# Kernel tuning notes

Hardware: AMD Instinct MI355X
Metric: run time of the kernel (lower is better)

The kernel has to match this reference:

```python
import jax, jax.numpy as jnp
import numpy as np

GRID = (32, 32)       # SOM grid shape
INPUT_DIM = 512
BATCH = 16384
TAU = 0.5             # softmax temperature
EPS = 1e-8


def setup_inputs() -> dict:
    key = jax.random.key(0)
    k1, k2 = jax.random.split(key)
    x = jax.random.normal(k1, (BATCH, INPUT_DIM), dtype=jnp.float32)
    # glorot_uniform for shape (*GRID, INPUT_DIM): fan_in = 32*32, fan_out = 512
    fan_in, fan_out = GRID[0] * GRID[1], INPUT_DIM
    limit = float(np.sqrt(6.0 / (fan_in + fan_out)))
    weights_map = jax.random.uniform(
        k2, (*GRID, INPUT_DIM), dtype=jnp.float32, minval=-limit, maxval=limit
    )
    return {"x": x, "weights_map": weights_map}


def reference(x, weights_map):
    """SoftSOM forward: squared distances -> per-dimension softmax -> soft reconstruction."""
    B, D = x.shape
    gh, gw = GRID
    w_flat = weights_map.reshape(gh * gw, D)  # [N, D]
    d2 = (
        jnp.sum(x * x, axis=-1, keepdims=True)           # [B,1]
        + jnp.sum(w_flat * w_flat, axis=-1)[None, :]     # [1,N]
        - 2.0 * (x @ w_flat.T)                           # [B,N]
    )
    logits = (-d2 / TAU).reshape(B, gh, gw)
    # per-dimension softmax: softmax along each grid axis, combined multiplicatively
    s_rows = jax.nn.softmax(logits, axis=1)   # softmax over grid dim 0
    s_cols = jax.nn.softmax(logits, axis=2)   # softmax over grid dim 1
    a = s_rows * s_cols
    a = a / (jnp.sum(a, axis=(1, 2), keepdims=True) + EPS)  # renormalize over grid
    # soft reconstruction: weighted sum of prototypes
    y = jnp.einsum("bij,ijd->bd", a, weights_map)  # [B, D]
    return y
```

## Files before the change

kernel.cpp:

```cpp
#include <hip/hip_runtime.h>
#include <hip/hip_bf16.h>
#include <stdint.h>

#define B_SZ 16384
#define D_SZ 512
#define N_SZ 1024

using f16x8 = __attribute__((ext_vector_type(8))) _Float16;
using f16x4 = __attribute__((ext_vector_type(4))) _Float16;
using f32x4 = __attribute__((ext_vector_type(4))) float;

typedef unsigned int u32_as1 __attribute__((address_space(1)));
typedef unsigned int u32_as3 __attribute__((address_space(3)));

__device__ __forceinline__ void gload16(const void* g, void* lds_base) {
    __builtin_amdgcn_global_load_lds((const u32_as1*)g, (u32_as3*)lds_base, 16, 0, 0);
}

__global__ __launch_bounds__(256) void prep(
    const float* __restrict__ W, const float* __restrict__ X,
    _Float16* __restrict__ wh, _Float16* __restrict__ wt,
    float* __restrict__ ww, _Float16* __restrict__ xh) {
    __shared__ float part[4];
    const int bid = blockIdx.x;
    const int t = threadIdx.x;
    if (bid < N_SZ) {
        const int n = bid;
        const float2 v = *reinterpret_cast<const float2*>(&W[(size_t)n * D_SZ + t * 2]);
        _Float16 h0 = (_Float16)v.x, h1 = (_Float16)v.y;
        wh[(size_t)n * D_SZ + t * 2] = h0;
        wh[(size_t)n * D_SZ + t * 2 + 1] = h1;
        wt[(size_t)(t * 2) * N_SZ + n] = h0;
        wt[(size_t)(t * 2 + 1) * N_SZ + n] = h1;
        float s = v.x * v.x + v.y * v.y;
        for (int o = 32; o; o >>= 1) s += __shfl_xor(s, o);
        if ((t & 63) == 0) part[t >> 6] = s;
        __syncthreads();
        if (t == 0) ww[n] = part[0] + part[1] + part[2] + part[3];
    } else {
        const int b2 = bid - N_SZ;
        const int chunk = (b2 & 7) * 512 + (b2 >> 3);
        const size_t idx = ((size_t)chunk * 256 + t) * 8;
        const float4 a = *reinterpret_cast<const float4*>(&X[idx]);
        const float4 b = *reinterpret_cast<const float4*>(&X[idx + 4]);
        f16x8 h = {(_Float16)a.x, (_Float16)a.y, (_Float16)a.z, (_Float16)a.w,
                   (_Float16)b.x, (_Float16)b.y, (_Float16)b.z, (_Float16)b.w};
        *reinterpret_cast<f16x8*>(&xh[idx]) = h;
    }
}

__global__ __launch_bounds__(256, 3) void gemm1(
    const _Float16* __restrict__ xh, const _Float16* __restrict__ wh,
    const float* __restrict__ ww, _Float16* __restrict__ L16) {
    __shared__ _Float16 smem[16384];
    const int tid = threadIdx.x;
    const int wid = tid >> 6, lane = tid & 63;
    const int raw = blockIdx.y * 8 + blockIdx.x;
    const int wsw = (raw & 7) * 128 + (raw >> 3);
    const int bn0 = (wsw & 7) * 128;
    const int bm0 = (wsw >> 3) * 128;
    const int m0 = (wid >> 1) * 64, n0 = (wid & 1) * 64;
    const int rA = lane & 15;
    const int cbr = (lane >> 4) * 16;
    const int rswz = ((rA >> 1) & 3) << 4;

    const int br0 = (wid * 2) * 16 + (lane >> 2);
    const int br1 = (wid * 2 + 1) * 16 + (lane >> 2);
    const int sg0 = ((lane & 3) ^ ((br0 >> 1) & 3)) * 8;
    const int sg1 = ((lane & 3) ^ ((br1 >> 1) & 3)) * 8;
    const int bdst0 = (wid * 2) * 1024;
    const int bdst1 = (wid * 2 + 1) * 1024;
    char* const As_b = (char*)smem;
    char* const Bs_b = (char*)smem + 16384;

    f32x4 acc[4][4];
    for (int mi = 0; mi < 4; ++mi)
        for (int ni = 0; ni < 4; ++ni) acc[mi][ni] = (f32x4){0.f, 0.f, 0.f, 0.f};

    gload16(&xh[(size_t)(bm0 + br0) * D_SZ + sg0], As_b + bdst0);
    gload16(&xh[(size_t)(bm0 + br1) * D_SZ + sg1], As_b + bdst1);
    gload16(&wh[(size_t)(bn0 + br0) * D_SZ + sg0], Bs_b + bdst0);
    gload16(&wh[(size_t)(bn0 + br1) * D_SZ + sg1], Bs_b + bdst1);
    __syncthreads();

    int cur = 0;
    for (int kt = 0; kt < 16; ++kt) {
        const int nxt = cur ^ 1;
        if (kt < 15) {
            const int gk = (kt + 1) * 32;
            gload16(&xh[(size_t)(bm0 + br0) * D_SZ + gk + sg0], As_b + nxt * 8192 + bdst0);
            gload16(&xh[(size_t)(bm0 + br1) * D_SZ + gk + sg1], As_b + nxt * 8192 + bdst1);
            gload16(&wh[(size_t)(bn0 + br0) * D_SZ + gk + sg0], Bs_b + nxt * 8192 + bdst0);
            gload16(&wh[(size_t)(bn0 + br1) * D_SZ + gk + sg1], Bs_b + nxt * 8192 + bdst1);
        }
        f16x8 af[4], bf[4];
        for (int mi = 0; mi < 4; ++mi)
            af[mi] = *reinterpret_cast<const f16x8*>(
                As_b + cur * 8192 + (m0 + mi * 16 + rA) * 64 + (cbr ^ rswz));
        for (int ni = 0; ni < 4; ++ni)
            bf[ni] = *reinterpret_cast<const f16x8*>(
                Bs_b + cur * 8192 + (n0 + ni * 16 + rA) * 64 + (cbr ^ rswz));
        for (int mi = 0; mi < 4; ++mi)
            for (int ni = 0; ni < 4; ++ni)
                acc[mi][ni] = __builtin_amdgcn_mfma_f32_16x16x32_f16(af[mi], bf[ni], acc[mi][ni], 0, 0, 0);
        __syncthreads();
        cur = nxt;
    }

    for (int mi = 0; mi < 4; ++mi)
        for (int ni = 0; ni < 4; ++ni) {
            const int ln = n0 + ni * 16 + rA;
            const float wwn = ww[bn0 + ln];
            const int lm = m0 + mi * 16 + (lane >> 4) * 4;
            const f32x4 a = acc[mi][ni];
            for (int r = 0; r < 4; ++r)
                smem[(lm + r) * 128 + ln] = (_Float16)(4.f * a[r] - 2.f * wwn);
        }
    __syncthreads();
    for (int c = 0; c < 8; ++c) {
        const int idx = c * 2048 + tid * 8;
        const int row = idx >> 7, col = idx & 127;
        const f16x8 v = *reinterpret_cast<const f16x8*>(&smem[idx]);
        *reinterpret_cast<f16x8*>(&L16[(size_t)(bm0 + row) * N_SZ + bn0 + col]) = v;
    }
}

__global__ __launch_bounds__(256) void softsm(_Float16* __restrict__ L16) {
    __shared__ float4 spart[4][8];
    __shared__ float mpart[4];
    __shared__ float Tp[4];
    const int t = threadIdx.x;
    const int w = t >> 6, lane = t & 63;
    const int g8 = t & 7;
    const int bid = blockIdx.x;
    const size_t row = (size_t)((bid & 7) * 2048 + (bid >> 3));
    const f16x4 lv = *reinterpret_cast<const f16x4*>(&L16[row * N_SZ + (size_t)t * 4]);
    const float v0 = (float)lv[0], v1 = (float)lv[1], v2 = (float)lv[2], v3 = (float)lv[3];

    float m = fmaxf(fmaxf(v0, v1), fmaxf(v2, v3));
    for (int o = 32; o; o >>= 1) m = fmaxf(m, __shfl_xor(m, o));
    if (lane == 0) mpart[w] = m;
    __syncthreads();
    m = fmaxf(fmaxf(mpart[0], mpart[1]), fmaxf(mpart[2], mpart[3]));

    const float u0 = __expf(v0 - m), u1 = __expf(v1 - m);
    const float u2 = __expf(v2 - m), u3 = __expf(v3 - m);
    float rs = (u0 + u1) + (u2 + u3);
    rs += __shfl_xor(rs, 1); rs += __shfl_xor(rs, 2); rs += __shfl_xor(rs, 4);
    float s0 = u0, s1 = u1, s2 = u2, s3 = u3;
    for (int o = 8; o <= 32; o <<= 1) {
        s0 += __shfl_xor(s0, o); s1 += __shfl_xor(s1, o);
        s2 += __shfl_xor(s2, o); s3 += __shfl_xor(s3, o);
    }
    if (lane < 8) spart[w][lane] = make_float4(s0, s1, s2, s3);
    __syncthreads();
    {
        const float4 q0 = spart[0][g8], q1 = spart[1][g8], q2 = spart[2][g8], q3 = spart[3][g8];
        s0 = (q0.x + q1.x) + (q2.x + q3.x);
        s1 = (q0.y + q1.y) + (q2.y + q3.y);
        s2 = (q0.z + q1.z) + (q2.z + q3.z);
        s3 = (q0.w + q1.w) + (q2.w + q3.w);
    }
    const float irs = __builtin_amdgcn_rcpf(rs);
    const float t0 = u0 * u0 * irs * __builtin_amdgcn_rcpf(s0);
    const float t1 = u1 * u1 * irs * __builtin_amdgcn_rcpf(s1);
    const float t2 = u2 * u2 * irs * __builtin_amdgcn_rcpf(s2);
    const float t3 = u3 * u3 * irs * __builtin_amdgcn_rcpf(s3);
    float sT = (t0 + t1) + (t2 + t3);
    for (int o = 1; o <= 32; o <<= 1) sT += __shfl_xor(sT, o);
    if (lane == 0) Tp[w] = sT;
    __syncthreads();
    const float T = (Tp[0] + Tp[1]) + (Tp[2] + Tp[3]);
    const float inv = __builtin_amdgcn_rcpf(T + 1e-8f);
    f16x4 o16 = {(_Float16)(t0 * inv), (_Float16)(t1 * inv),
                 (_Float16)(t2 * inv), (_Float16)(t3 * inv)};
    *reinterpret_cast<f16x4*>(&L16[row * N_SZ + (size_t)t * 4]) = o16;
}

__global__ __launch_bounds__(256, 3) void gemm2(
    const _Float16* __restrict__ a16, const _Float16* __restrict__ wt,
    float* __restrict__ Y) {
    __shared__ _Float16 As[2 * 128 * 32];
    __shared__ _Float16 Bs[2 * 128 * 32];
    const int tid = threadIdx.x;
    const int wid = tid >> 6, lane = tid & 63;
    const int raw = blockIdx.y * 4 + blockIdx.x;
    const int wsw = (raw & 7) * 64 + (raw >> 3);
    const int bn0 = (wsw & 3) * 128;
    const int bm0 = (wsw >> 2) * 128;
    const int m0 = (wid >> 1) * 64, n0 = (wid & 1) * 64;
    const int rA = lane & 15;
    const int cbr = (lane >> 4) * 16;
    const int rswz = ((rA >> 1) & 3) << 4;

    const int br0 = (wid * 2) * 16 + (lane >> 2);
    const int br1 = (wid * 2 + 1) * 16 + (lane >> 2);
    const int sg0 = ((lane & 3) ^ ((br0 >> 1) & 3)) * 8;
    const int sg1 = ((lane & 3) ^ ((br1 >> 1) & 3)) * 8;
    const int bdst0 = (wid * 2) * 1024;
    const int bdst1 = (wid * 2 + 1) * 1024;
    char* const As_b = (char*)As;
    char* const Bs_b = (char*)Bs;

    f32x4 acc[4][4];
    for (int mi = 0; mi < 4; ++mi)
        for (int ni = 0; ni < 4; ++ni) acc[mi][ni] = (f32x4){0.f, 0.f, 0.f, 0.f};

    gload16(&a16[(size_t)(bm0 + br0) * N_SZ + sg0], As_b + bdst0);
    gload16(&a16[(size_t)(bm0 + br1) * N_SZ + sg1], As_b + bdst1);
    gload16(&wt[(size_t)(bn0 + br0) * N_SZ + sg0], Bs_b + bdst0);
    gload16(&wt[(size_t)(bn0 + br1) * N_SZ + sg1], Bs_b + bdst1);
    __syncthreads();

    int cur = 0;
    for (int kt = 0; kt < 32; ++kt) {
        const int nxt = cur ^ 1;
        if (kt < 31) {
            const int gk = (kt + 1) * 32;
            gload16(&a16[(size_t)(bm0 + br0) * N_SZ + gk + sg0], As_b + nxt * 8192 + bdst0);
            gload16(&a16[(size_t)(bm0 + br1) * N_SZ + gk + sg1], As_b + nxt * 8192 + bdst1);
            gload16(&wt[(size_t)(bn0 + br0) * N_SZ + gk + sg0], Bs_b + nxt * 8192 + bdst0);
            gload16(&wt[(size_t)(bn0 + br1) * N_SZ + gk + sg1], Bs_b + nxt * 8192 + bdst1);
        }
        f16x8 af[4], bf[4];
        for (int mi = 0; mi < 4; ++mi)
            af[mi] = *reinterpret_cast<const f16x8*>(
                As_b + cur * 8192 + (m0 + mi * 16 + rA) * 64 + (cbr ^ rswz));
        for (int ni = 0; ni < 4; ++ni)
            bf[ni] = *reinterpret_cast<const f16x8*>(
                Bs_b + cur * 8192 + (n0 + ni * 16 + rA) * 64 + (cbr ^ rswz));
        for (int mi = 0; mi < 4; ++mi)
            for (int ni = 0; ni < 4; ++ni)
                acc[mi][ni] = __builtin_amdgcn_mfma_f32_16x16x32_f16(af[mi], bf[ni], acc[mi][ni], 0, 0, 0);
        __syncthreads();
        cur = nxt;
    }
    for (int mi = 0; mi < 4; ++mi)
        for (int ni = 0; ni < 4; ++ni) {
            const int dd = bn0 + n0 + ni * 16 + rA;
            const int bb = bm0 + m0 + mi * 16 + (lane >> 4) * 4;
            const f32x4 a = acc[mi][ni];
            for (int r = 0; r < 4; ++r)
                Y[(size_t)(bb + r) * D_SZ + dd] = a[r];
        }
}

extern "C" void kernel_launch(void* const* d_in, const int* in_sizes, int n_in,
                              void* d_out, int out_size, void* d_ws, size_t ws_size,
                              hipStream_t stream) {
    (void)in_sizes; (void)n_in; (void)out_size; (void)ws_size;
    const float* X = (const float*)d_in[0];
    const float* W = (const float*)d_in[1];
    float* Y = (float*)d_out;
    char* ws = (char*)d_ws;

    _Float16* L16 = (_Float16*)ws;
    _Float16* wh  = (_Float16*)(ws + (size_t)32 * 1024 * 1024);
    _Float16* wt  = (_Float16*)(ws + (size_t)33 * 1024 * 1024);
    float*    ww  = (float*)   (ws + (size_t)34 * 1024 * 1024);
    _Float16* xh  = (_Float16*)(ws + (size_t)34 * 1024 * 1024 + 4096);

    prep<<<N_SZ + 4096, 256, 0, stream>>>(W, X, wh, wt, ww, xh);
    gemm1<<<dim3(N_SZ / 128, B_SZ / 128), 256, 0, stream>>>(xh, wh, ww, L16);
    softsm<<<B_SZ, 256, 0, stream>>>(L16);
    gemm2<<<dim3(D_SZ / 128, B_SZ / 128), 256, 0, stream>>>(L16, wt, Y);
}
```

Measured before the change: 99.54 us.

## Tile weight transpose through LDS, process two rows per softmax block, raise occupancy

The weight prep path now uses 32 blocks, each covering 32 prototypes. Each block computes the squared norms, writes the fp16 copy with 16-byte stores, and transposes through padded, swizzled LDS so the transposed weights are also written with coalesced 16-byte stores instead of scattered 2-byte writes. The softmax kernel handles two rows per 512-thread block, which halves the block count. Both GEMMs raise their launch-bounds occupancy hint from 3 to 4 blocks, which may force register spills.

```diff
diff --git a/kernel.cpp b/kernel.cpp
--- a/kernel.cpp
+++ b/kernel.cpp
@@ -15,30 +15,79 @@
 
 __device__ __forceinline__ void gload16(const void* g, void* lds_base) {
     __builtin_amdgcn_global_load_lds((const u32_as1*)g, (u32_as3*)lds_base, 16, 0, 0);
+}
+
+__device__ __forceinline__ unsigned short f16bits(_Float16 h) {
+    return __builtin_bit_cast(unsigned short, h);
 }
 
 __global__ __launch_bounds__(256) void prep(
     const float* __restrict__ W, const float* __restrict__ X,
     _Float16* __restrict__ wh, _Float16* __restrict__ wt,
     float* __restrict__ ww, _Float16* __restrict__ xh) {
-    __shared__ float part[4];
     const int bid = blockIdx.x;
     const int t = threadIdx.x;
-    if (bid < N_SZ) {
-        const int n = bid;
-        const float2 v = *reinterpret_cast<const float2*>(&W[(size_t)n * D_SZ + t * 2]);
-        _Float16 h0 = (_Float16)v.x, h1 = (_Float16)v.y;
-        wh[(size_t)n * D_SZ + t * 2] = h0;
-        wh[(size_t)n * D_SZ + t * 2 + 1] = h1;
-        wt[(size_t)(t * 2) * N_SZ + n] = h0;
-        wt[(size_t)(t * 2 + 1) * N_SZ + n] = h1;
-        float s = v.x * v.x + v.y * v.y;
-        for (int o = 32; o; o >>= 1) s += __shfl_xor(s, o);
-        if ((t & 63) == 0) part[t >> 6] = s;
+    if (bid < 32) {
+        __shared__ unsigned int cells[512 * 17];
+        const int n0 = bid * 32;
+        const int np = t >> 4;
+        const int dc = t & 15;
+        const int na = n0 + 2 * np, nb = na + 1;
+        const int d0 = dc * 32;
+        float va[32], vb[32];
+#pragma unroll
+        for (int i = 0; i < 8; ++i) {
+            *reinterpret_cast<float4*>(&va[i * 4]) =
+                *reinterpret_cast<const float4*>(&W[(size_t)na * D_SZ + d0 + i * 4]);
+            *reinterpret_cast<float4*>(&vb[i * 4]) =
+                *reinterpret_cast<const float4*>(&W[(size_t)nb * D_SZ + d0 + i * 4]);
+        }
+        float sa = 0.f, sb = 0.f;
+#pragma unroll
+        for (int i = 0; i < 32; ++i) { sa += va[i] * va[i]; sb += vb[i] * vb[i]; }
+        sa += __shfl_xor(sa, 1); sa += __shfl_xor(sa, 2);
+        sa += __shfl_xor(sa, 4); sa += __shfl_xor(sa, 8);
+        sb += __shfl_xor(sb, 1); sb += __shfl_xor(sb, 2);
+        sb += __shfl_xor(sb, 4); sb += __shfl_xor(sb, 8);
+        if (dc == 0) { ww[na] = sa; ww[nb] = sb; }
+        _Float16 ha[32], hb[32];
+#pragma unroll
+        for (int i = 0; i < 32; ++i) { ha[i] = (_Float16)va[i]; hb[i] = (_Float16)vb[i]; }
+        unsigned int pa[16], pb[16];
+#pragma unroll
+        for (int j = 0; j < 16; ++j) {
+            pa[j] = (unsigned)f16bits(ha[2 * j]) | ((unsigned)f16bits(ha[2 * j + 1]) << 16);
+            pb[j] = (unsigned)f16bits(hb[2 * j]) | ((unsigned)f16bits(hb[2 * j + 1]) << 16);
+        }
+        unsigned int* whU = reinterpret_cast<unsigned int*>(wh);
+#pragma unroll
+        for (int j = 0; j < 4; ++j) {
+            *reinterpret_cast<uint4*>(&whU[((size_t)na * D_SZ + d0) / 2 + j * 4]) =
+                make_uint4(pa[j * 4], pa[j * 4 + 1], pa[j * 4 + 2], pa[j * 4 + 3]);
+            *reinterpret_cast<uint4*>(&whU[((size_t)nb * D_SZ + d0) / 2 + j * 4]) =
+                make_uint4(pb[j * 4], pb[j * 4 + 1], pb[j * 4 + 2], pb[j * 4 + 3]);
+        }
+#pragma unroll
+        for (int k = 0; k < 32; ++k) {
+            const int d = d0 + k;
+            const unsigned u = (unsigned)f16bits(ha[k]) | ((unsigned)f16bits(hb[k]) << 16);
+            cells[d * 17 + (np ^ ((d >> 5) & 15))] = u;
+        }
         __syncthreads();
-        if (t == 0) ww[n] = part[0] + part[1] + part[2] + part[3];
+        for (int rr = 0; rr < 2; ++rr) {
+            const int d = 2 * t + rr;
+            const int px = (d >> 5) & 15;
+            unsigned int buf[16];
+#pragma unroll
+            for (int j = 0; j < 16; ++j) buf[j] = cells[d * 17 + (j ^ px)];
+            unsigned int* wtU = reinterpret_cast<unsigned int*>(wt);
+#pragma unroll
+            for (int j = 0; j < 4; ++j)
+                *reinterpret_cast<uint4*>(&wtU[((size_t)d * N_SZ + n0) / 2 + j * 4]) =
+                    make_uint4(buf[j * 4], buf[j * 4 + 1], buf[j * 4 + 2], buf[j * 4 + 3]);
+        }
     } else {
-        const int b2 = bid - N_SZ;
+        const int b2 = bid - 32;
         const int chunk = (b2 & 7) * 512 + (b2 >> 3);
         const size_t idx = ((size_t)chunk * 256 + t) * 8;
         const float4 a = *reinterpret_cast<const float4*>(&X[idx]);
@@ -49,7 +98,7 @@
     }
 }
 
-__global__ __launch_bounds__(256, 3) void gemm1(
+__global__ __launch_bounds__(256, 4) void gemm1(
     const _Float16* __restrict__ xh, const _Float16* __restrict__ wh,
     const float* __restrict__ ww, _Float16* __restrict__ L16) {
     __shared__ _Float16 smem[16384];
@@ -125,23 +174,24 @@
     }
 }
 
-__global__ __launch_bounds__(256) void softsm(_Float16* __restrict__ L16) {
-    __shared__ float4 spart[4][8];
-    __shared__ float mpart[4];
-    __shared__ float Tp[4];
-    const int t = threadIdx.x;
+__global__ __launch_bounds__(512) void softsm(_Float16* __restrict__ L16) {
+    __shared__ float4 spart[2][4][8];
+    __shared__ float mpart[2][4];
+    __shared__ float Tp[2][4];
+    const int h = threadIdx.x >> 8;
+    const int t = threadIdx.x & 255;
     const int w = t >> 6, lane = t & 63;
     const int g8 = t & 7;
     const int bid = blockIdx.x;
-    const size_t row = (size_t)((bid & 7) * 2048 + (bid >> 3));
+    const size_t row = (size_t)(bid & 7) * 2048 + (size_t)(bid >> 3) * 2 + h;
     const f16x4 lv = *reinterpret_cast<const f16x4*>(&L16[row * N_SZ + (size_t)t * 4]);
     const float v0 = (float)lv[0], v1 = (float)lv[1], v2 = (float)lv[2], v3 = (float)lv[3];
 
     float m = fmaxf(fmaxf(v0, v1), fmaxf(v2, v3));
     for (int o = 32; o; o >>= 1) m = fmaxf(m, __shfl_xor(m, o));
-    if (lane == 0) mpart[w] = m;
-    __syncthreads();
-    m = fmaxf(fmaxf(mpart[0], mpart[1]), fmaxf(mpart[2], mpart[3]));
+    if (lane == 0) mpart[h][w] = m;
+    __syncthreads();
+    m = fmaxf(fmaxf(mpart[h][0], mpart[h][1]), fmaxf(mpart[h][2], mpart[h][3]));
 
     const float u0 = __expf(v0 - m), u1 = __expf(v1 - m);
     const float u2 = __expf(v2 - m), u3 = __expf(v3 - m);
@@ -152,10 +202,11 @@
         s0 += __shfl_xor(s0, o); s1 += __shfl_xor(s1, o);
         s2 += __shfl_xor(s2, o); s3 += __shfl_xor(s3, o);
     }
-    if (lane < 8) spart[w][lane] = make_float4(s0, s1, s2, s3);
+    if (lane < 8) spart[h][w][lane] = make_float4(s0, s1, s2, s3);
     __syncthreads();
     {
-        const float4 q0 = spart[0][g8], q1 = spart[1][g8], q2 = spart[2][g8], q3 = spart[3][g8];
+        const float4 q0 = spart[h][0][g8], q1 = spart[h][1][g8];
+        const float4 q2 = spart[h][2][g8], q3 = spart[h][3][g8];
         s0 = (q0.x + q1.x) + (q2.x + q3.x);
         s1 = (q0.y + q1.y) + (q2.y + q3.y);
         s2 = (q0.z + q1.z) + (q2.z + q3.z);
@@ -168,16 +219,16 @@
     const float t3 = u3 * u3 * irs * __builtin_amdgcn_rcpf(s3);
     float sT = (t0 + t1) + (t2 + t3);
     for (int o = 1; o <= 32; o <<= 1) sT += __shfl_xor(sT, o);
-    if (lane == 0) Tp[w] = sT;
-    __syncthreads();
-    const float T = (Tp[0] + Tp[1]) + (Tp[2] + Tp[3]);
+    if (lane == 0) Tp[h][w] = sT;
+    __syncthreads();
+    const float T = (Tp[h][0] + Tp[h][1]) + (Tp[h][2] + Tp[h][3]);
     const float inv = __builtin_amdgcn_rcpf(T + 1e-8f);
     f16x4 o16 = {(_Float16)(t0 * inv), (_Float16)(t1 * inv),
                  (_Float16)(t2 * inv), (_Float16)(t3 * inv)};
     *reinterpret_cast<f16x4*>(&L16[row * N_SZ + (size_t)t * 4]) = o16;
 }
 
-__global__ __launch_bounds__(256, 3) void gemm2(
+__global__ __launch_bounds__(256, 4) void gemm2(
     const _Float16* __restrict__ a16, const _Float16* __restrict__ wt,
     float* __restrict__ Y) {
     __shared__ _Float16 As[2 * 128 * 32];
@@ -260,8 +311,8 @@
     float*    ww  = (float*)   (ws + (size_t)34 * 1024 * 1024);
     _Float16* xh  = (_Float16*)(ws + (size_t)34 * 1024 * 1024 + 4096);
 
-    prep<<<N_SZ + 4096, 256, 0, stream>>>(W, X, wh, wt, ww, xh);
+    prep<<<32 + 4096, 256, 0, stream>>>(W, X, wh, wt, ww, xh);
     gemm1<<<dim3(N_SZ / 128, B_SZ / 128), 256, 0, stream>>>(xh, wh, ww, L16);
-    softsm<<<B_SZ, 256, 0, stream>>>(L16);
+    softsm<<<B_SZ / 2, 512, 0, stream>>>(L16);
     gemm2<<<dim3(D_SZ / 128, B_SZ / 128), 256, 0, stream>>>(L16, wt, Y);
 }
```

Result: no change. 99.46 us (median of 3 runs) (-0.1%).
